# Optimization experiments

Hardware: AMD Instinct MI355X
Metric: run time of the kernel (lower is better)

Reference implementation:

```python
import jax, jax.numpy as jnp
import numpy as np

H = 1024   # hidden_dim
NH = 16    # num_heads
HD = H // NH  # head_dim = 64
B, S = 2, 2048
LN_EPS = 1e-5


def setup_inputs() -> dict:
    key = jax.random.key(0)
    ks = jax.random.split(key, 5)
    scale = 1.0 / np.sqrt(H)  # xavier-ish scale for stability
    return {
        "x": jax.random.normal(ks[0], (B, S, H), dtype=jnp.float32),
        "Wq": jax.random.normal(ks[1], (H, H), dtype=jnp.float32) * scale,
        "bq": jnp.zeros((H,), jnp.float32),
        "Wk": jax.random.normal(ks[2], (H, H), dtype=jnp.float32) * scale,
        "bk": jnp.zeros((H,), jnp.float32),
        "Wv": jax.random.normal(ks[3], (H, H), dtype=jnp.float32) * scale,
        "bv": jnp.zeros((H,), jnp.float32),
        "Wo": jax.random.normal(ks[4], (H, H), dtype=jnp.float32) * scale,
        "bo": jnp.zeros((H,), jnp.float32),
        "ln_gamma": jnp.ones((H,), jnp.float32),
        "ln_beta": jnp.zeros((H,), jnp.float32),
    }


def reference(x, Wq, bq, Wk, bk, Wv, bv, Wo, bo, ln_gamma, ln_beta):
    b, s, _ = x.shape
    # QKV projections, split heads: (b, nh, s, hd)
    def split_heads(t):
        return t.reshape(b, s, NH, HD).transpose(0, 2, 1, 3)
    Q = split_heads(x @ Wq + bq)
    K = split_heads(x @ Wk + bk)
    V = split_heads(x @ Wv + bv)
    # scaled dot-product with clamp (mask=None path)
    scores = jnp.einsum('bhqd,bhkd->bhqk', Q, K) / np.sqrt(HD).astype(np.float32)
    scores = jnp.clip(scores, -10000.0, 10000.0)
    attn = jax.nn.softmax(scores, axis=-1)
    # dropout is identity in eval mode
    ctx = jnp.einsum('bhqk,bhkd->bhqd', attn, V)
    ctx = ctx.transpose(0, 2, 1, 3).reshape(b, s, H)
    out = ctx @ Wo + bo
    # residual + LayerNorm
    y = out + x
    mu = jnp.mean(y, axis=-1, keepdims=True)
    var = jnp.mean(jnp.square(y - mu), axis=-1, keepdims=True)
    y = (y - mu) * jax.lax.rsqrt(var + LN_EPS)
    return y * ln_gamma + ln_beta
```

## Files before the change

kernel.cpp:

```cpp
#include <hip/hip_runtime.h>

typedef unsigned short u16;
typedef __attribute__((ext_vector_type(8))) short shortx8;
typedef __attribute__((ext_vector_type(4))) float floatx4;
typedef __attribute__((ext_vector_type(2))) float floatx2;
typedef __attribute__((ext_vector_type(2))) unsigned uintx2;
typedef __attribute__((ext_vector_type(4))) unsigned uintx4;

#define GLD16(gp, lp) __builtin_amdgcn_global_load_lds( \
    (__attribute__((address_space(1))) void*)(gp), \
    (__attribute__((address_space(3))) void*)(lp), 16, 0, 0)

#define BAR() __builtin_amdgcn_s_barrier()
#define LGKM0() do { asm volatile("s_waitcnt lgkmcnt(0)" ::: "memory"); \
                     __builtin_amdgcn_sched_barrier(0); } while (0)
#define VMCNT0() do { asm volatile("s_waitcnt vmcnt(0)" ::: "memory"); \
                      __builtin_amdgcn_sched_barrier(0); } while (0)

__device__ __forceinline__ u16 f2bf(float f) {
  union { float f; unsigned u; } v; v.f = f;
  unsigned r = v.u + 0x7FFFu + ((v.u >> 16) & 1u);
  return (u16)(r >> 16);
}

__device__ __forceinline__ unsigned pkbf(float a, float b) {
#if __has_builtin(__builtin_amdgcn_cvt_pk_bf16_f32)
  auto r = __builtin_amdgcn_cvt_pk_bf16_f32(a, b);
  return __builtin_bit_cast(unsigned, r);
#else
  union { float f; unsigned u; } x, y; x.f = a; y.f = b;
  return __builtin_amdgcn_perm(y.u + 0x8000u, x.u + 0x8000u, 0x07060302u);
#endif
}

__global__ __launch_bounds__(256) void prep_kernel(const float* __restrict__ x,
                                                   u16* __restrict__ xb,
                                                   const float* __restrict__ Wq,
                                                   const float* __restrict__ Wk,
                                                   const float* __restrict__ Wv,
                                                   const float* __restrict__ Wo,
                                                   u16* __restrict__ Wt) {
  __shared__ u16 tile[32][33];
  int bid = blockIdx.x;
  int tid = threadIdx.x;
  if (bid < 4096) {
    int i = bid * 256 + tid;
    float4 v = ((const float4*)x)[i];
    uintx2 o;
    o.x = pkbf(v.x, v.y);
    o.y = pkbf(v.z, v.w);
    ((uintx2*)xb)[i] = o;
  } else {
    int block = bid - 4096;
    int mat = block >> 10;
    int rem = block & 1023;
    const float* W = (mat == 0) ? Wq : (mat == 1) ? Wk : (mat == 2) ? Wv : Wo;
    u16* dst = Wt + (size_t)mat * 1024 * 1024;
    int n0 = (rem & 31) * 32, k0 = (rem >> 5) * 32;
    int tx = tid & 31, ty = tid >> 5;
    for (int i = 0; i < 4; ++i)
      tile[ty + i * 8][tx] = f2bf(W[(size_t)(k0 + ty + i * 8) * 1024 + n0 + tx]);
    __syncthreads();
    for (int i = 0; i < 4; ++i)
      dst[(size_t)(n0 + ty + i * 8) * 1024 + k0 + tx] = tile[tx][ty + i * 8];
  }
}

__global__ __launch_bounds__(512, 1) void qkv_gemm(const u16* __restrict__ xb,
                                                   const u16* __restrict__ Wt,
                                                   const float* __restrict__ bq,
                                                   const float* __restrict__ bk,
                                                   const float* __restrict__ bv,
                                                   u16* __restrict__ Qh,
                                                   u16* __restrict__ Kh,
                                                   u16* __restrict__ Vth) {
  __shared__ u16 lds[65536];
  const int tid = threadIdx.x;
  const int wave = tid >> 6, lane = tid & 63;
  const int lrow = lane >> 4, lcol = lane & 15;
  const int wm = wave >> 2, wn = wave & 3;
  const int m0 = blockIdx.x * 256;
  const int n0 = blockIdx.y * 192;
  const u16* Ag = xb;
  const u16* Bg = Wt;

  const u16* sa[4];
  const u16* sb[3];
#pragma unroll
  for (int l = 0; l < 4; ++l) {
    int g = (l * 8 + wave) * 64 + lane;
    int r = g >> 3, c = g & 7;
    sa[l] = Ag + (size_t)(m0 + r) * 1024 + ((c ^ (r & 7)) * 8);
  }
#pragma unroll
  for (int l = 0; l < 3; ++l) {
    int g = (l * 8 + wave) * 64 + lane;
    int r = g >> 3, c = g & 7;
    sb[l] = Bg + (size_t)(n0 + r) * 1024 + ((c ^ (r & 7)) * 8);
  }

  floatx4 acc[8][3];
#pragma unroll
  for (int mi = 0; mi < 8; ++mi)
#pragma unroll
    for (int ni = 0; ni < 3; ++ni)
      acc[mi][ni] = (floatx4){0.f, 0.f, 0.f, 0.f};

#pragma unroll
  for (int l = 0; l < 4; ++l) GLD16(sa[l], lds + (l * 8 + wave) * 512);
#pragma unroll
  for (int l = 0; l < 3; ++l) GLD16(sb[l], lds + 16384 + (l * 8 + wave) * 512);
  VMCNT0();
  BAR();

#pragma unroll 2
  for (int t = 0; t < 16; ++t) {
    const int rb = t & 1, wb = rb ^ 1;
    const u16* Ab = lds + rb * 28672;
    const u16* Bb = lds + rb * 28672 + 16384;
    u16* Aw = lds + wb * 28672;
    u16* Bw = lds + wb * 28672 + 16384;
    const int k64 = (t + 1) * 64;

    if (t < 15) {
#pragma unroll
      for (int l = 0; l < 4; ++l) GLD16(sa[l] + k64, Aw + (l * 8 + wave) * 512);
    }
    shortx8 bfr[3][2];
#pragma unroll
    for (int ni = 0; ni < 3; ++ni) {
      int rn = wn * 48 + ni * 16 + lcol;
#pragma unroll
      for (int kk = 0; kk < 2; ++kk)
        bfr[ni][kk] = *(const shortx8*)&Bb[rn * 64 + (((kk * 4 + lrow) ^ (rn & 7)) * 8)];
    }
    {
      shortx8 afr[2][2];
#pragma unroll
      for (int j = 0; j < 2; ++j) {
        int rm = wm * 128 + j * 16 + lcol;
#pragma unroll
        for (int kk = 0; kk < 2; ++kk)
          afr[j][kk] = *(const shortx8*)&Ab[rm * 64 + (((kk * 4 + lrow) ^ (rm & 7)) * 8)];
      }
      BAR();
      LGKM0();
      __builtin_amdgcn_s_setprio(1);
#pragma unroll
      for (int kk = 0; kk < 2; ++kk)
#pragma unroll
        for (int j = 0; j < 2; ++j)
#pragma unroll
          for (int ni = 0; ni < 3; ++ni)
            acc[j][ni] = __builtin_amdgcn_mfma_f32_16x16x32_bf16(
                afr[j][kk], bfr[ni][kk], acc[j][ni], 0, 0, 0);
      __builtin_amdgcn_s_setprio(0);
      BAR();
    }
    if (t < 15) {
#pragma unroll
      for (int l = 0; l < 3; ++l) GLD16(sb[l] + k64, Bw + (l * 8 + wave) * 512);
    }
    {
      shortx8 afr[2][2];
#pragma unroll
      for (int j = 0; j < 2; ++j) {
        int rm = wm * 128 + (2 + j) * 16 + lcol;
#pragma unroll
        for (int kk = 0; kk < 2; ++kk)
          afr[j][kk] = *(const shortx8*)&Ab[rm * 64 + (((kk * 4 + lrow) ^ (rm & 7)) * 8)];
      }
      BAR();
      LGKM0();
      __builtin_amdgcn_s_setprio(1);
#pragma unroll
      for (int kk = 0; kk < 2; ++kk)
#pragma unroll
        for (int j = 0; j < 2; ++j)
#pragma unroll
          for (int ni = 0; ni < 3; ++ni)
            acc[2 + j][ni] = __builtin_amdgcn_mfma_f32_16x16x32_bf16(
                afr[j][kk], bfr[ni][kk], acc[2 + j][ni], 0, 0, 0);
      __builtin_amdgcn_s_setprio(0);
      BAR();
    }
    {
      shortx8 afr[2][2];
#pragma unroll
      for (int j = 0; j < 2; ++j) {
        int rm = wm * 128 + (4 + j) * 16 + lcol;
#pragma unroll
        for (int kk = 0; kk < 2; ++kk)
          afr[j][kk] = *(const shortx8*)&Ab[rm * 64 + (((kk * 4 + lrow) ^ (rm & 7)) * 8)];
      }
      BAR();
      LGKM0();
      __builtin_amdgcn_s_setprio(1);
#pragma unroll
      for (int kk = 0; kk < 2; ++kk)
#pragma unroll
        for (int j = 0; j < 2; ++j)
#pragma unroll
          for (int ni = 0; ni < 3; ++ni)
            acc[4 + j][ni] = __builtin_amdgcn_mfma_f32_16x16x32_bf16(
                afr[j][kk], bfr[ni][kk], acc[4 + j][ni], 0, 0, 0);
      __builtin_amdgcn_s_setprio(0);
      BAR();
    }
    {
      shortx8 afr[2][2];
#pragma unroll
      for (int j = 0; j < 2; ++j) {
        int rm = wm * 128 + (6 + j) * 16 + lcol;
#pragma unroll
        for (int kk = 0; kk < 2; ++kk)
          afr[j][kk] = *(const shortx8*)&Ab[rm * 64 + (((kk * 4 + lrow) ^ (rm & 7)) * 8)];
      }
      BAR();
      LGKM0();
      __builtin_amdgcn_s_setprio(1);
#pragma unroll
      for (int kk = 0; kk < 2; ++kk)
#pragma unroll
        for (int j = 0; j < 2; ++j)
#pragma unroll
          for (int ni = 0; ni < 3; ++ni)
            acc[6 + j][ni] = __builtin_amdgcn_mfma_f32_16x16x32_bf16(
                afr[j][kk], bfr[ni][kk], acc[6 + j][ni], 0, 0, 0);
      __builtin_amdgcn_s_setprio(0);
      VMCNT0();
      BAR();
    }
  }

  const float qscale = 0.18033688011f;
  __syncthreads();

#pragma unroll
  for (int mi = 0; mi < 8; ++mi) {
    int mb = wm * 128 + mi * 16 + lrow * 4;
#pragma unroll
    for (int ni = 0; ni < 3; ++ni) {
      int nl = wn * 48 + ni * 16 + lcol;
      int ng = n0 + nl;
      int mt = ng >> 10;
      if (mt < 2) {
        float sc = (mt == 0) ? qscale : 1.0f;
        float bval = ((mt == 0) ? bq : bk)[ng & 1023] * sc;
#pragma unroll
        for (int r = 0; r < 4; ++r) {
          int m = mb + r;
          lds[m * 256 + (((nl >> 3) ^ (m & 31)) * 8) + (nl & 7)] =
              f2bf(acc[mi][ni][r] * sc + bval);
        }
      } else {
        float bval = bv[ng & 1023];
        int mbase = m0 + mb;
        int bb = mbase >> 11, s = mbase & 2047;
        int hh = (ng & 1023) >> 6, d = ng & 63;
        uintx2 pk;
        pk.x = pkbf(acc[mi][ni][0] + bval, acc[mi][ni][1] + bval);
        pk.y = pkbf(acc[mi][ni][2] + bval, acc[mi][ni][3] + bval);
        *(uintx2*)&Vth[((size_t)(bb * 16 + hh) * 64 + d) * 2048 + s] = pk;
      }
    }
  }
  __syncthreads();
  {
    int row = tid >> 1, half = tid & 1;
    int m = m0 + row;
    int bb = m >> 11, s = m & 2047;
#pragma unroll
    for (int i = 0; i < 12; ++i) {
      int cg = half * 12 + i;
      int ng = n0 + cg * 8;
      int mt = ng >> 10;
      if (mt >= 2) continue;
      u16* dst = (mt == 0) ? Qh : Kh;
      int pg = cg ^ (row & 31);
      shortx8 v = *(const shortx8*)&lds[row * 256 + pg * 8];
      int hh = (ng & 1023) >> 6, d = ng & 63;
      *(shortx8*)&dst[((size_t)(bb * 16 + hh) * 2048 + s) * 64 + d] = v;
    }
  }
}

__global__ __launch_bounds__(256, 2) void out_gemm(const u16* __restrict__ ctx,
                                                   const u16* __restrict__ Wot,
                                                   const float* __restrict__ bo,
                                                   float* __restrict__ aout) {
  __shared__ u16 lds[24576];
  const int tid = threadIdx.x;
  const int wave = tid >> 6, lane = tid & 63;
  const int lrow = lane >> 4, lcol = lane & 15;
  const int wm = wave >> 1, wn = wave & 1;
  const int m0 = blockIdx.x * 128;
  const int n0 = blockIdx.y * 64;

  const u16* sa[4];
  const u16* sb[2];
#pragma unroll
  for (int l = 0; l < 4; ++l) {
    int g = (l * 4 + wave) * 64 + lane;
    int r = g >> 3, c = g & 7;
    sa[l] = ctx + (size_t)(m0 + r) * 1024 + ((c ^ (r & 7)) * 8);
  }
#pragma unroll
  for (int l = 0; l < 2; ++l) {
    int g = (l * 4 + wave) * 64 + lane;
    int r = g >> 3, c = g & 7;
    sb[l] = Wot + (size_t)(n0 + r) * 1024 + ((c ^ (r & 7)) * 8);
  }

  floatx4 acc[4][2];
#pragma unroll
  for (int mi = 0; mi < 4; ++mi)
#pragma unroll
    for (int ni = 0; ni < 2; ++ni)
      acc[mi][ni] = (floatx4){0.f, 0.f, 0.f, 0.f};

#pragma unroll
  for (int l = 0; l < 4; ++l) GLD16(sa[l], lds + (l * 4 + wave) * 512);
#pragma unroll
  for (int l = 0; l < 2; ++l) GLD16(sb[l], lds + 8192 + (l * 4 + wave) * 512);
  VMCNT0();
  BAR();

#pragma unroll 2
  for (int t = 0; t < 16; ++t) {
    const int rb = t & 1, wb = rb ^ 1;
    const u16* Ab = lds + rb * 12288;
    const u16* Bb = lds + rb * 12288 + 8192;
    u16* Aw = lds + wb * 12288;
    u16* Bw = lds + wb * 12288 + 8192;
    const int k64 = (t + 1) * 64;

    if (t < 15) {
#pragma unroll
      for (int l = 0; l < 4; ++l) GLD16(sa[l] + k64, Aw + (l * 4 + wave) * 512);
    }
    shortx8 bfr[2][2];
#pragma unroll
    for (int ni = 0; ni < 2; ++ni) {
      int rn = wn * 32 + ni * 16 + lcol;
#pragma unroll
      for (int kk = 0; kk < 2; ++kk)
        bfr[ni][kk] = *(const shortx8*)&Bb[rn * 64 + (((kk * 4 + lrow) ^ (rn & 7)) * 8)];
    }
    {
      shortx8 afr[2][2];
#pragma unroll
      for (int j = 0; j < 2; ++j) {
        int rm = wm * 64 + j * 16 + lcol;
#pragma unroll
        for (int kk = 0; kk < 2; ++kk)
          afr[j][kk] = *(const shortx8*)&Ab[rm * 64 + (((kk * 4 + lrow) ^ (rm & 7)) * 8)];
      }
      BAR();
      LGKM0();
      __builtin_amdgcn_s_setprio(1);
#pragma unroll
      for (int kk = 0; kk < 2; ++kk)
#pragma unroll
        for (int j = 0; j < 2; ++j)
#pragma unroll
          for (int ni = 0; ni < 2; ++ni)
            acc[j][ni] = __builtin_amdgcn_mfma_f32_16x16x32_bf16(
                afr[j][kk], bfr[ni][kk], acc[j][ni], 0, 0, 0);
      __builtin_amdgcn_s_setprio(0);
      BAR();
    }
    if (t < 15) {
#pragma unroll
      for (int l = 0; l < 2; ++l) GLD16(sb[l] + k64, Bw + (l * 4 + wave) * 512);
    }
    {
      shortx8 afr[2][2];
#pragma unroll
      for (int j = 0; j < 2; ++j) {
        int rm = wm * 64 + (2 + j) * 16 + lcol;
#pragma unroll
        for (int kk = 0; kk < 2; ++kk)
          afr[j][kk] = *(const shortx8*)&Ab[rm * 64 + (((kk * 4 + lrow) ^ (rm & 7)) * 8)];
      }
      BAR();
      LGKM0();
      __builtin_amdgcn_s_setprio(1);
#pragma unroll
      for (int kk = 0; kk < 2; ++kk)
#pragma unroll
        for (int j = 0; j < 2; ++j)
#pragma unroll
          for (int ni = 0; ni < 2; ++ni)
            acc[2 + j][ni] = __builtin_amdgcn_mfma_f32_16x16x32_bf16(
                afr[j][kk], bfr[ni][kk], acc[2 + j][ni], 0, 0, 0);
      __builtin_amdgcn_s_setprio(0);
      VMCNT0();
      BAR();
    }
  }

#pragma unroll
  for (int mi = 0; mi < 4; ++mi) {
    int mbase = m0 + wm * 64 + mi * 16 + lrow * 4;
#pragma unroll
    for (int ni = 0; ni < 2; ++ni) {
      int n = n0 + wn * 32 + ni * 16 + lcol;
      float bval = bo[n];
#pragma unroll
      for (int r = 0; r < 4; ++r)
        aout[(size_t)(mbase + r) * 1024 + n] = acc[mi][ni][r] + bval;
    }
  }
}

__global__ __launch_bounds__(512) void attn_kernel(const u16* __restrict__ Qh,
                                                   const u16* __restrict__ Kh,
                                                   const u16* __restrict__ Vth,
                                                   u16* __restrict__ ctx) {
  __shared__ u16 QPs[128 * 64];
  __shared__ u16 Ks[2][64 * 64];
  __shared__ u16 Vs[2][64 * 64];

  int bh = blockIdx.x;
  int b = bh >> 4, h = bh & 15;
  int q0 = blockIdx.y * 128;
  int tid = threadIdx.x;
  int wave = tid >> 6, lane = tid & 63;
  int lrow = lane >> 4, lcol = lane & 15;

  const u16* Qg = Qh + ((size_t)bh * 2048 + q0) * 64;
  for (int l = 0; l < 2; ++l) {
    int g = (l * 8 + wave) * 64 + lane;
    int r = g >> 3, c = g & 7;
    GLD16(Qg + r * 64 + ((c ^ (r & 7)) * 8), QPs + (l * 8 + wave) * 512);
  }

  const u16* Kbase = Kh + (size_t)bh * 2048 * 64;
  const u16* Vbase = Vth + (size_t)bh * 64 * 2048;

  int g = wave * 64 + lane;
  int gr = g >> 3, gc = g & 7;
  int cc = (gc ^ (gr & 7)) * 8;
  const u16* kp = Kbase + (size_t)gr * 64 + cc;

  const u16* vp = Vbase + (size_t)gr * 2048 + gc * 8;
  int hh = gc >> 2, ct = gc & 3;
  int ua = 4 * (ct & 1) + (ct >> 1);
  int chunkA = hh * 4 + (ua >> 1);
  int offA = gr * 128 + ((chunkA ^ (gr & 7)) * 16) + (ua & 1) * 8;
  int offB = gr * 128 + (((chunkA + 1) ^ (gr & 7)) * 16) + (ua & 1) * 8;

  {
    float4 vreg = *(const float4*)vp;
    vp += 64;
    GLD16(kp, (u16*)Ks + wave * 512);
    kp += 4096;
    char* vb = (char*)Vs;
    *(floatx2*)(vb + offA) = (floatx2){vreg.x, vreg.y};
    *(floatx2*)(vb + offB) = (floatx2){vreg.z, vreg.w};
  }
  __syncthreads();

  shortx8 qf[2];
  for (int kk = 0; kk < 2; ++kk) {
    int row = wave * 16 + lcol;
    int grr = (kk * 4 + lrow) ^ (row & 7);
    qf[kk] = *(const shortx8*)&QPs[row * 64 + grr * 8];
  }

  const short one_bf = (short)0x3F80;
  const shortx8 ones8 = {one_bf, one_bf, one_bf, one_bf, one_bf, one_bf, one_bf, one_bf};

  floatx4 o[4];
  floatx4 lacc = (floatx4){0.f, 0.f, 0.f, 0.f};
  for (int dt = 0; dt < 4; ++dt) o[dt] = (floatx4){0.f, 0.f, 0.f, 0.f};

  for (int i = 0; i < 32; ++i) {
    int cur = i & 1;
    float4 vreg;
    if (i < 31) {
      vreg = *(const float4*)vp;
      vp += 64;
      GLD16(kp, (u16*)Ks + (cur ^ 1) * 4096 + wave * 512);
      kp += 4096;
    }

    floatx4 sc[4];
    for (int kt = 0; kt < 4; ++kt)
      sc[kt] = (floatx4){0.f, 0.f, 0.f, 0.f};
    __builtin_amdgcn_s_setprio(1);
    for (int kk = 0; kk < 2; ++kk) {
      for (int kt = 0; kt < 4; ++kt) {
        int row = kt * 16 + lcol;
        int grr = (kk * 4 + lrow) ^ (row & 7);
        shortx8 kf = *(const shortx8*)&Ks[cur][row * 64 + grr * 8];
        sc[kt] = __builtin_amdgcn_mfma_f32_16x16x32_bf16(kf, qf[kk], sc[kt], 0, 0, 0);
      }
    }
    __builtin_amdgcn_s_setprio(0);

    float p[4][4];
    for (int kt = 0; kt < 4; ++kt)
      for (int r = 0; r < 4; ++r)
        p[kt][r] = __builtin_amdgcn_exp2f(sc[kt][r]);
    shortx8 pf[2];
    for (int kk = 0; kk < 2; ++kk) {
      uintx4 w;
      w.x = pkbf(p[2 * kk][0], p[2 * kk][1]);
      w.y = pkbf(p[2 * kk][2], p[2 * kk][3]);
      w.z = pkbf(p[2 * kk + 1][0], p[2 * kk + 1][1]);
      w.w = pkbf(p[2 * kk + 1][2], p[2 * kk + 1][3]);
      pf[kk] = __builtin_bit_cast(shortx8, w);
    }

    if (i < 31) {
      char* vb = (char*)Vs + (cur ^ 1) * 8192;
      *(floatx2*)(vb + offA) = (floatx2){vreg.x, vreg.y};
      *(floatx2*)(vb + offB) = (floatx2){vreg.z, vreg.w};
    }

    __builtin_amdgcn_s_setprio(1);
    for (int kk = 0; kk < 2; ++kk) {
      lacc = __builtin_amdgcn_mfma_f32_16x16x32_bf16(ones8, pf[kk], lacc, 0, 0, 0);
      for (int dt = 0; dt < 4; ++dt) {
        int row = dt * 16 + lcol;
        int grr = (kk * 4 + lrow) ^ (row & 7);
        shortx8 vf = *(const shortx8*)&Vs[cur][row * 64 + grr * 8];
        o[dt] = __builtin_amdgcn_mfma_f32_16x16x32_bf16(vf, pf[kk], o[dt], 0, 0, 0);
      }
    }
    __builtin_amdgcn_s_setprio(0);
    __syncthreads();
  }

  {
    float inv = 1.0f / lacc[0];
    int s = q0 + wave * 16 + lcol;
    u16* dst = ctx + (size_t)(b * 2048 + s) * 1024 + h * 64 + lrow * 4;
    for (int dt = 0; dt < 4; ++dt) {
      uintx2 pk;
      pk.x = pkbf(o[dt][0] * inv, o[dt][1] * inv);
      pk.y = pkbf(o[dt][2] * inv, o[dt][3] * inv);
      *(uintx2*)(dst + dt * 16) = pk;
    }
  }
}

__global__ __launch_bounds__(256) void ln_kernel(const float* __restrict__ aout,
                                                 const float* __restrict__ x,
                                                 const float* __restrict__ gamma,
                                                 const float* __restrict__ beta,
                                                 float* __restrict__ out) {
  int row = blockIdx.x;
  int t = threadIdx.x;
  const float4* a4 = (const float4*)(aout + (size_t)row * 1024);
  const float4* x4 = (const float4*)(x + (size_t)row * 1024);
  float4 v = a4[t];
  float4 xv = x4[t];
  v.x += xv.x; v.y += xv.y; v.z += xv.z; v.w += xv.w;
  float s = v.x + v.y + v.z + v.w;
  float s2 = v.x * v.x + v.y * v.y + v.z * v.z + v.w * v.w;
  for (int off = 1; off < 64; off <<= 1) {
    s += __shfl_xor(s, off, 64);
    s2 += __shfl_xor(s2, off, 64);
  }
  __shared__ float red[8];
  int wave = t >> 6, lane = t & 63;
  if (lane == 0) { red[wave] = s; red[4 + wave] = s2; }
  __syncthreads();
  s = red[0] + red[1] + red[2] + red[3];
  s2 = red[4] + red[5] + red[6] + red[7];
  float mu = s * (1.0f / 1024.0f);
  float var = s2 * (1.0f / 1024.0f) - mu * mu;
  float rstd = rsqrtf(var + 1e-5f);
  float4 g = ((const float4*)gamma)[t];
  float4 be = ((const float4*)beta)[t];
  float4 y;
  y.x = (v.x - mu) * rstd * g.x + be.x;
  y.y = (v.y - mu) * rstd * g.y + be.y;
  y.z = (v.z - mu) * rstd * g.z + be.z;
  y.w = (v.w - mu) * rstd * g.w + be.w;
  ((float4*)(out + (size_t)row * 1024))[t] = y;
}

extern "C" void kernel_launch(void* const* d_in, const int* in_sizes, int n_in,
                              void* d_out, int out_size, void* d_ws, size_t ws_size,
                              hipStream_t stream) {
  const float* x     = (const float*)d_in[0];
  const float* Wq    = (const float*)d_in[1];
  const float* bq    = (const float*)d_in[2];
  const float* Wk    = (const float*)d_in[3];
  const float* bk    = (const float*)d_in[4];
  const float* Wv    = (const float*)d_in[5];
  const float* bv    = (const float*)d_in[6];
  const float* Wo    = (const float*)d_in[7];
  const float* bo    = (const float*)d_in[8];
  const float* gamma = (const float*)d_in[9];
  const float* beta  = (const float*)d_in[10];
  float* out = (float*)d_out;

  char* ws = (char*)d_ws;
  u16* xb   = (u16*)(ws);
  u16* Wt   = (u16*)(ws + ((size_t)8 << 20));
  u16* Qh   = (u16*)(ws + ((size_t)16 << 20));
  u16* Kh   = (u16*)(ws + ((size_t)24 << 20));
  u16* Vth  = (u16*)(ws + ((size_t)32 << 20));
  u16* ctx  = (u16*)(ws + ((size_t)40 << 20));
  float* aout = (float*)(ws + ((size_t)48 << 20));

  prep_kernel<<<8192, 256, 0, stream>>>(x, xb, Wq, Wk, Wv, Wo, Wt);
  qkv_gemm<<<dim3(16, 16), 512, 0, stream>>>(xb, Wt, bq, bk, bv, Qh, Kh, Vth);
  attn_kernel<<<dim3(32, 16), 512, 0, stream>>>(Qh, Kh, Vth, ctx);
  out_gemm<<<dim3(32, 16), 256, 0, stream>>>(ctx, Wt + (size_t)3 * 1024 * 1024, bo, aout);
  ln_kernel<<<4096, 256, 0, stream>>>(aout, x, gamma, beta, out);
}
```

Before: 195.5 us.

## Triple-buffer A tiles in QKV GEMM to prefetch two K-steps ahead

The QKV GEMM's shared-memory pipeline becomes three-stage for the A (activation) tiles and stays double-buffered for B. A tiles are prefetched two iterations ahead, and each iteration ends with a partial vmcnt wait instead of a full drain. The goal is to keep global loads in flight across iteration boundaries and hide load latency behind MFMA work. In exchange, LDS use grows to 144KB, the loop is no longer unrolled, and the modulo-3 buffer indexing adds address arithmetic.

```diff
diff --git a/kernel.cpp b/kernel.cpp
--- a/kernel.cpp
+++ b/kernel.cpp
@@ -15,6 +15,8 @@
 #define LGKM0() do { asm volatile("s_waitcnt lgkmcnt(0)" ::: "memory"); \
                      __builtin_amdgcn_sched_barrier(0); } while (0)
 #define VMCNT0() do { asm volatile("s_waitcnt vmcnt(0)" ::: "memory"); \
+                      __builtin_amdgcn_sched_barrier(0); } while (0)
+#define VMCNT4() do { asm volatile("s_waitcnt vmcnt(4)" ::: "memory"); \
                       __builtin_amdgcn_sched_barrier(0); } while (0)
 
 __device__ __forceinline__ u16 f2bf(float f) {
@@ -74,7 +76,7 @@
                                                    u16* __restrict__ Qh,
                                                    u16* __restrict__ Kh,
                                                    u16* __restrict__ Vth) {
-  __shared__ u16 lds[65536];
+  __shared__ u16 lds[73728];
   const int tid = threadIdx.x;
   const int wave = tid >> 6, lane = tid & 63;
   const int lrow = lane >> 4, lcol = lane & 15;
@@ -84,14 +86,16 @@
   const u16* Ag = xb;
   const u16* Bg = Wt;
 
-  const u16* sa[4];
+  const u16* sa[2][2];
+#pragma unroll
+  for (int h = 0; h < 2; ++h)
+#pragma unroll
+    for (int l = 0; l < 2; ++l) {
+      int g = (l * 8 + wave) * 64 + lane;
+      int r = g >> 3, c = g & 7;
+      sa[h][l] = Ag + (size_t)(m0 + h * 128 + r) * 1024 + ((c ^ (r & 7)) * 8);
+    }
   const u16* sb[3];
-#pragma unroll
-  for (int l = 0; l < 4; ++l) {
-    int g = (l * 8 + wave) * 64 + lane;
-    int r = g >> 3, c = g & 7;
-    sa[l] = Ag + (size_t)(m0 + r) * 1024 + ((c ^ (r & 7)) * 8);
-  }
 #pragma unroll
   for (int l = 0; l < 3; ++l) {
     int g = (l * 8 + wave) * 64 + lane;
@@ -99,6 +103,23 @@
     sb[l] = Bg + (size_t)(n0 + r) * 1024 + ((c ^ (r & 7)) * 8);
   }
 
+  auto stageA = [&](int t) {
+    u16* d = lds + (t % 3) * 16384;
+    int k64 = t * 64;
+#pragma unroll
+    for (int h = 0; h < 2; ++h)
+#pragma unroll
+      for (int l = 0; l < 2; ++l)
+        GLD16(sa[h][l] + k64, d + h * 8192 + (l * 8 + wave) * 512);
+  };
+  auto stageB = [&](int t) {
+    u16* d = lds + 49152 + (t & 1) * 12288;
+    int k64 = t * 64;
+#pragma unroll
+    for (int l = 0; l < 3; ++l)
+      GLD16(sb[l] + k64, d + (l * 8 + wave) * 512);
+  };
+
   floatx4 acc[8][3];
 #pragma unroll
   for (int mi = 0; mi < 8; ++mi)
@@ -106,26 +127,18 @@
     for (int ni = 0; ni < 3; ++ni)
       acc[mi][ni] = (floatx4){0.f, 0.f, 0.f, 0.f};
 
-#pragma unroll
-  for (int l = 0; l < 4; ++l) GLD16(sa[l], lds + (l * 8 + wave) * 512);
-#pragma unroll
-  for (int l = 0; l < 3; ++l) GLD16(sb[l], lds + 16384 + (l * 8 + wave) * 512);
-  VMCNT0();
+  stageA(0);
+  stageB(0);
+  stageA(1);
+  VMCNT4();
   BAR();
 
-#pragma unroll 2
+#pragma unroll 1
   for (int t = 0; t < 16; ++t) {
-    const int rb = t & 1, wb = rb ^ 1;
-    const u16* Ab = lds + rb * 28672;
-    const u16* Bb = lds + rb * 28672 + 16384;
-    u16* Aw = lds + wb * 28672;
-    u16* Bw = lds + wb * 28672 + 16384;
-    const int k64 = (t + 1) * 64;
-
-    if (t < 15) {
-#pragma unroll
-      for (int l = 0; l < 4; ++l) GLD16(sa[l] + k64, Aw + (l * 8 + wave) * 512);
-    }
+    const u16* Ab = lds + (t % 3) * 16384;
+    const u16* Bb = lds + 49152 + (t & 1) * 12288;
+
+    if (t < 15) stageB(t + 1);
     shortx8 bfr[3][2];
 #pragma unroll
     for (int ni = 0; ni < 3; ++ni) {
@@ -157,10 +170,7 @@
       __builtin_amdgcn_s_setprio(0);
       BAR();
     }
-    if (t < 15) {
-#pragma unroll
-      for (int l = 0; l < 3; ++l) GLD16(sb[l] + k64, Bw + (l * 8 + wave) * 512);
-    }
+    if (t < 14) stageA(t + 2);
     {
       shortx8 afr[2][2];
 #pragma unroll
@@ -228,7 +238,11 @@
             acc[6 + j][ni] = __builtin_amdgcn_mfma_f32_16x16x32_bf16(
                 afr[j][kk], bfr[ni][kk], acc[6 + j][ni], 0, 0, 0);
       __builtin_amdgcn_s_setprio(0);
-      VMCNT0();
+      if (t < 14) {
+        VMCNT4();
+      } else if (t == 14) {
+        VMCNT0();
+      }
       BAR();
     }
   }
```

Result: no change. 194.2 us (-0.7%).
